# Optimization experiments

Hardware: AMD Instinct MI355X
Metric: run time of the kernel (lower is better)

The kernel has to match this reference:

```python
import jax, jax.numpy as jnp
import numpy as np

NUM_EMB = 8192
EMB_DIM = 512
SPAN = 8            # max_span == fixed_segment_size
COMMIT = 0.25
BOUND_W = 0.01


def setup_inputs() -> dict:
    key = jax.random.key(0)
    k_x, k_e, k_w = jax.random.split(key, 3)
    B, T, D = 16, 8192, EMB_DIM
    x = jax.random.normal(k_x, (B, T, D), dtype=jnp.float32)
    emb = jax.random.normal(k_e, (NUM_EMB, D), dtype=jnp.float32) * 0.02
    Wb = jax.random.normal(k_w, (D, 1), dtype=jnp.float32) * 0.02
    bb = jnp.zeros((1,), dtype=jnp.float32)
    return {"x": x, "emb": emb, "Wb": Wb, "bb": bb}


def reference(x, emb, Wb, bb):
    # Eval-mode forward of AdaptiveTemporalVQ (no gumbel sampling, no EMA update).
    B, T, D = x.shape
    # boundary predictor: Linear(D, 1) -> squeeze
    boundary_logits = (x @ Wb)[..., 0] + bb[0]                      # [B, T]
    boundaries = (jax.nn.sigmoid(boundary_logits) > 0.5).astype(x.dtype)

    num_segments = (T + SPAN - 1) // SPAN
    pad = num_segments * SPAN - T
    x_p = jnp.pad(x, ((0, 0), (0, pad), (0, 0))) if pad > 0 else x
    # temporal mean pooling over fixed segments
    pooled = x_p.reshape(B, num_segments, SPAN, D).mean(axis=2)      # [B, S, D]

    # --- VectorQuantizer ---
    flat = pooled.reshape(-1, D)                                     # [N, D]
    dist = (jnp.sum(flat ** 2, axis=1, keepdims=True)
            + jnp.sum(emb ** 2, axis=1)
            - 2.0 * flat @ emb.T)                                    # [N, K]
    idx = jnp.argmin(dist, axis=1)                                   # [N]
    quantized = emb[idx].reshape(B, num_segments, D)                 # codebook gather

    e_latent_loss = jnp.mean((jax.lax.stop_gradient(quantized) - pooled) ** 2)
    vq_loss = COMMIT * e_latent_loss
    # straight-through estimator
    q_st = pooled + jax.lax.stop_gradient(quantized - pooled)

    # expand each segment code back over its SPAN timesteps
    q_exp = jnp.broadcast_to(q_st[:, :, None, :], (B, num_segments, SPAN, D))
    quantized_out = q_exp.reshape(B, num_segments * SPAN, D)[:, :T, :]
    idx_seg = idx.reshape(B, num_segments)
    idx_out = jnp.broadcast_to(idx_seg[:, :, None], (B, num_segments, SPAN))
    idx_out = idx_out.reshape(B, num_segments * SPAN)[:, :T]

    target_rate = jnp.float32(1.0 / SPAN)
    boundary_loss = (boundaries.mean() - target_rate) ** 2
    total_loss = vq_loss + BOUND_W * boundary_loss
    return quantized_out, total_loss, idx_out, boundaries
```

## Files before the change

kernel.cpp:

```cpp
#include <hip/hip_runtime.h>

#define B_    16
#define T_    8192
#define D_    512
#define K_    8192
#define S_    1024
#define N_    16384
#define NBT   131072

#define LOSS_OFF 67108864
#define IDX_OFF  67108865
#define BND_OFF  67239937

typedef __bf16 bf16x8 __attribute__((ext_vector_type(8)));
typedef float  f32x4  __attribute__((ext_vector_type(4)));

__device__ __forceinline__ unsigned int fsort(float f){
  unsigned int u = __float_as_uint(f);
  return (u & 0x80000000u) ? ~u : (u | 0x80000000u);
}
__device__ __forceinline__ float funsort(unsigned int su){
  unsigned int u = (su & 0x80000000u) ? (su ^ 0x80000000u) : ~su;
  return __uint_as_float(u);
}
__device__ __forceinline__ unsigned short f2bf(float f){
  unsigned int u = __float_as_uint(f);
  return (unsigned short)((u + 0x7fffu + ((u >> 16) & 1u)) >> 16);
}
__device__ __forceinline__ void gload16(const void* g, void* l){
  __builtin_amdgcn_global_load_lds((const __attribute__((address_space(1))) void*)g,
                                   (__attribute__((address_space(3))) void*)l, 16, 0, 0);
}

__global__ void k_init(int* cnt){
  if(threadIdx.x == 0 && blockIdx.x == 0) *cnt = 0;
}

__global__ void k_embnorm(const float4* __restrict__ emb4, float* __restrict__ enorm,
                          unsigned short* __restrict__ embh){
  const int wid  = (blockIdx.x * blockDim.x + threadIdx.x) >> 6;
  const int lane = threadIdx.x & 63;
  float4 a = emb4[wid * 128 + (lane << 1)];
  float4 b = emb4[wid * 128 + (lane << 1) + 1];
  float s = a.x*a.x + a.y*a.y + a.z*a.z + a.w*a.w
          + b.x*b.x + b.y*b.y + b.z*b.z + b.w*b.w;
  #pragma unroll
  for(int off = 32; off; off >>= 1) s += __shfl_xor(s, off);
  if(lane == 0) enorm[wid] = s;
  unsigned short* dst = embh + ((size_t)wid << 9) + (lane << 3);
  *(ushort4*)(dst)     = make_ushort4(f2bf(a.x), f2bf(a.y), f2bf(a.z), f2bf(a.w));
  *(ushort4*)(dst + 4) = make_ushort4(f2bf(b.x), f2bf(b.y), f2bf(b.z), f2bf(b.w));
}

__launch_bounds__(256)
__global__ void k_prep(const float4* __restrict__ x4, const float4* __restrict__ wb4,
                       const float* __restrict__ bb, float4* __restrict__ pooled4,
                       unsigned short* __restrict__ pooledh, float* __restrict__ bnd,
                       int* __restrict__ cnt){
  __shared__ double ld[4][8][8];
  const int tid  = threadIdx.x;
  const int row0 = blockIdx.x << 5;
  const double bbv = (double)bb[0];
  #pragma unroll
  for(int it = 0; it < 2; it++){
    const int slot  = (it << 8) + tid;
    const int seg_l = slot >> 7;
    const int c4    = slot & 127;
    const float4 w  = wb4[c4];
    const float4* src = x4 + ((size_t)(row0 + (seg_l << 3)) * 128 + c4);
    float4 acc = src[0];
    double p[8];
    p[0] = (double)acc.x*w.x + (double)acc.y*w.y + (double)acc.z*w.z + (double)acc.w*w.w;
    #pragma unroll
    for(int t = 1; t < 8; t++){
      const float4 v = src[(size_t)t * 128];
      acc.x += v.x; acc.y += v.y; acc.z += v.z; acc.w += v.w;
      p[t] = (double)v.x*w.x + (double)v.y*w.y + (double)v.z*w.z + (double)v.w*w.w;
    }
    acc.x *= 0.125f; acc.y *= 0.125f; acc.z *= 0.125f; acc.w *= 0.125f;
    const int u = ((blockIdx.x << 2) + seg_l) * 128 + c4;
    pooled4[u] = acc;
    *(ushort4*)(pooledh + ((size_t)u << 2)) =
        make_ushort4(f2bf(acc.x), f2bf(acc.y), f2bf(acc.z), f2bf(acc.w));
    #pragma unroll
    for(int t = 0; t < 8; t++){
      #pragma unroll
      for(int off = 1; off < 16; off <<= 1) p[t] += __shfl_xor(p[t], off);
    }
    if((c4 & 15) == 0){
      #pragma unroll
      for(int t = 0; t < 8; t++) ld[seg_l][t][c4 >> 4] = p[t];
    }
  }
  __syncthreads();
  if(tid < 32){
    const double* q = ld[tid >> 3][tid & 7];
    double s = bbv;
    #pragma unroll
    for(int h = 0; h < 8; h++) s += q[h];
    const bool f = s > 0.0;
    bnd[row0 + tid] = f ? 1.0f : 0.0f;
    const unsigned long long m = __ballot(f);
    if(tid == 0) atomicAdd(cnt, (int)__popcll(m));
  }
}

__launch_bounds__(256, 4)
__global__ void k_distx(const unsigned short* __restrict__ Ah,
                        const unsigned short* __restrict__ Bh,
                        const float* __restrict__ enorm,
                        unsigned long long* __restrict__ cand64){
  __shared__ __align__(16) unsigned short sA[4096];
  __shared__ __align__(16) unsigned short sB[4096];
  const int tid  = threadIdx.x;
  const int w    = tid >> 6, lane = tid & 63;
  const int wm   = w >> 1,  wn   = w & 1;
  const int c    = lane & 15, q  = lane >> 4;

  const int bid   = blockIdx.x;
  const int st    = bid >> 9;
  const int loc   = bid & 511;
  const int row_t = (st << 3) + (loc & 7);
  const int col_t = loc >> 3;
  const int rowbase = row_t << 7;
  const int colbase = col_t << 7;

  f32x4 acc[4][4];
  #pragma unroll
  for(int i = 0; i < 4; i++)
    #pragma unroll
    for(int j = 0; j < 4; j++) acc[i][j] = (f32x4){0.f, 0.f, 0.f, 0.f};

  const int sr  = lane >> 2;
  const int skc = (lane & 3) << 3;

  const unsigned short* Ap0 = Ah + (size_t)(rowbase + w*32 + sr)      * 512 + skc;
  const unsigned short* Ap1 = Ah + (size_t)(rowbase + w*32 + 16 + sr) * 512 + skc;
  const unsigned short* Bp0 = Bh + (size_t)(colbase + w*32 + sr)      * 512 + skc;
  const unsigned short* Bp1 = Bh + (size_t)(colbase + w*32 + 16 + sr) * 512 + skc;
  unsigned short* lA0 = &sA[(w*32)      * 32];
  unsigned short* lA1 = &sA[(w*32 + 16) * 32];
  unsigned short* lB0 = &sB[(w*32)      * 32];
  unsigned short* lB1 = &sB[(w*32 + 16) * 32];

  for(int kb = 0; kb < 512; kb += 32){
    gload16(Ap0 + kb, lA0);
    gload16(Ap1 + kb, lA1);
    gload16(Bp0 + kb, lB0);
    gload16(Bp1 + kb, lB1);
    __syncthreads();
    bf16x8 af[4], bg[4];
    #pragma unroll
    for(int i = 0; i < 4; i++) af[i] = *(const bf16x8*)&sA[(wm*64 + i*16 + c)*32 + q*8];
    #pragma unroll
    for(int j = 0; j < 4; j++) bg[j] = *(const bf16x8*)&sB[(wn*64 + j*16 + c)*32 + q*8];
    #pragma unroll
    for(int i = 0; i < 4; i++)
      #pragma unroll
      for(int j = 0; j < 4; j++)
        acc[i][j] = __builtin_amdgcn_mfma_f32_16x16x32_bf16(af[i], bg[j], acc[i][j], 0, 0, 0);
    __syncthreads();
  }

  float en[4];
  #pragma unroll
  for(int j = 0; j < 4; j++) en[j] = enorm[colbase + wn*64 + j*16 + c];

  #pragma unroll
  for(int i = 0; i < 4; i++){
    #pragma unroll
    for(int r = 0; r < 4; r++){
      unsigned int k1 = 0xffffffffu, k2 = 0xffffffffu;
      #pragma unroll
      for(int j = 0; j < 4; j++){
        const float d = fmaf(-2.0f, acc[i][j][r], en[j]);
        const unsigned int col = (unsigned int)(colbase + wn*64 + j*16 + c);
        const unsigned int key = (fsort(d) & 0xffffe000u) | col;
        if(key < k1){ k2 = k1; k1 = key; } else if(key < k2){ k2 = key; }
      }
      #pragma unroll
      for(int off = 1; off < 4; off <<= 1){
        const unsigned int o1 = __shfl_xor(k1, off);
        const unsigned int o2 = __shfl_xor(k2, off);
        if(o1 < k1){ k2 = min(k1, o2); k1 = o1; }
        else       { k2 = min(k2, o1); }
      }
      if((c & 3) == 0){
        const int row = rowbase + wm*64 + i*16 + (q << 2) + r;
        const int g   = (col_t << 3) + (wn << 2) + (c >> 2);
        cand64[(size_t)row * 512 + g] = ((unsigned long long)k2 << 32) | k1;
      }
    }
  }
}

__launch_bounds__(256)
__global__ void k_fixup(const float* __restrict__ pooled, const float* __restrict__ emb,
                        const unsigned int* __restrict__ cand,
                        int* __restrict__ idxf, double* __restrict__ part){
  const int lane = threadIdx.x & 63, wv = threadIdx.x >> 6;
  const int row = (blockIdx.x << 2) + wv;
  const uint4* cr = (const uint4*)(cand + ((size_t)row << 10));
  unsigned int ks[16];
  #pragma unroll
  for(int m = 0; m < 4; m++){
    const uint4 v = cr[m*64 + lane];
    ks[m*4+0] = v.x; ks[m*4+1] = v.y; ks[m*4+2] = v.z; ks[m*4+3] = v.w;
  }
  unsigned int mn = 0xffffffffu;
  #pragma unroll
  for(int g = 0; g < 16; g++) mn = min(mn, ks[g]);
  #pragma unroll
  for(int off = 32; off; off >>= 1) mn = min(mn, (unsigned int)__shfl_xor(mn, off));
  const float thr = funsort(mn & 0xffffe000u) + 0.01f;

  double bestd = 1e300; int besti = 0x7fffffff;
  const float4* p4 = (const float4*)(pooled + ((size_t)row << 9));
  const float4 pa = p4[lane << 1], pb = p4[(lane << 1) + 1];
  #pragma unroll
  for(int g = 0; g < 16; g++){
    const bool flag = funsort(ks[g] & 0xffffe000u) <= thr;
    unsigned long long mask = __ballot(flag);
    while(mask){
      const int l = __ffsll(mask) - 1;
      mask &= mask - 1;
      const int code = (int)(__shfl(ks[g], l) & 0x1fffu);
      const float4* e4 = (const float4*)(emb + ((size_t)code << 9));
      const float4 ea = e4[lane << 1], eb = e4[(lane << 1) + 1];
      double s = 0.0, d;
      d = (double)pa.x - ea.x; s += d * d;  d = (double)pa.y - ea.y; s += d * d;
      d = (double)pa.z - ea.z; s += d * d;  d = (double)pa.w - ea.w; s += d * d;
      d = (double)pb.x - eb.x; s += d * d;  d = (double)pb.y - eb.y; s += d * d;
      d = (double)pb.z - eb.z; s += d * d;  d = (double)pb.w - eb.w; s += d * d;
      #pragma unroll
      for(int off = 32; off; off >>= 1) s += __shfl_xor(s, off);
      if(s < bestd || (s == bestd && code < besti)){ bestd = s; besti = code; }
    }
  }
  __shared__ double se[4];
  if(lane == 0){ idxf[row] = besti; se[wv] = bestd; }
  __syncthreads();
  if(threadIdx.x == 0) part[blockIdx.x] = se[0] + se[1] + se[2] + se[3];
}

__global__ void k_loss(const double* __restrict__ part, const int* __restrict__ cnt,
                       float* __restrict__ out_loss){
  const int tid = threadIdx.x;
  double s = 0.0;
  for(int i = tid; i < 4096; i += 256) s += part[i];
  #pragma unroll
  for(int off = 32; off; off >>= 1) s += __shfl_xor(s, off);
  __shared__ double sb[4];
  if((tid & 63) == 0) sb[tid >> 6] = s;
  __syncthreads();
  if(tid == 0){
    const double e  = sb[0] + sb[1] + sb[2] + sb[3];
    const double el = e / (double)((size_t)N_ * 512);
    const double bm = (double)(*cnt) / 131072.0 - 0.125;
    const double loss = 0.25 * el + 0.01 * bm * bm;
    *out_loss = (float)loss;
  }
}

__launch_bounds__(256)
__global__ void k_expand(const float4* __restrict__ emb4, const int* __restrict__ idxf,
                         float4* __restrict__ q4, float* __restrict__ idxo){
  const int lane = threadIdx.x & 63, wv = threadIdx.x >> 6;
  const int seg = (blockIdx.x << 2) + wv;
  const int idx = idxf[seg];
  const float4 a = emb4[idx * 128 + (lane << 1)];
  const float4 b = emb4[idx * 128 + (lane << 1) + 1];
  float4* dst = q4 + ((size_t)seg << 10);
  #pragma unroll
  for(int t = 0; t < 8; t++){
    dst[t * 128 + (lane << 1)]     = a;
    dst[t * 128 + (lane << 1) + 1] = b;
  }
  if(lane < 8) idxo[(seg << 3) + lane] = (float)idx;
}

extern "C" void kernel_launch(void* const* d_in, const int* in_sizes, int n_in,
                              void* d_out, int out_size, void* d_ws, size_t ws_size,
                              hipStream_t stream){
  const float* x   = (const float*)d_in[0];
  const float* emb = (const float*)d_in[1];
  const float* wb  = (const float*)d_in[2];
  const float* bb  = (const float*)d_in[3];
  float* out = (float*)d_out;

  char* ws = (char*)d_ws;
  int*    cnt   = (int*)(ws + 0);
  double* part  = (double*)(ws + 64);
  float*  enorm = (float*)(ws + 32832);
  int*    idxf  = (int*)(ws + 65600);

  float*              pooled  = (float*)d_out;
  unsigned long long* cand64  = (unsigned long long*)((char*)d_out + (48ull  << 20));
  unsigned short*     pooledh = (unsigned short*)((char*)d_out + (112ull << 20));
  unsigned short*     embh    = (unsigned short*)((char*)d_out + (128ull << 20));

  float* bnd   = out + BND_OFF;
  float* idxo  = out + IDX_OFF;
  float* lossp = out + LOSS_OFF;

  hipLaunchKernelGGL(k_init,    dim3(1),     dim3(64),  0, stream, cnt);
  hipLaunchKernelGGL(k_embnorm, dim3(2048),  dim3(256), 0, stream, (const float4*)emb, enorm, embh);
  hipLaunchKernelGGL(k_prep,    dim3(4096),  dim3(256), 0, stream, (const float4*)x, (const float4*)wb,
                     bb, (float4*)pooled, pooledh, bnd, cnt);
  hipLaunchKernelGGL(k_distx,   dim3(8192),  dim3(256), 0, stream, pooledh, embh, enorm, cand64);
  hipLaunchKernelGGL(k_fixup,   dim3(4096),  dim3(256), 0, stream, pooled, emb, (const unsigned int*)cand64, idxf, part);
  hipLaunchKernelGGL(k_loss,    dim3(1),     dim3(256), 0, stream, part, cnt, lossp);
  hipLaunchKernelGGL(k_expand,  dim3(4096),  dim3(256), 0, stream, (const float4*)emb, idxf, (float4*)d_out, idxo);
}
```

Measured before the change: 702.0 us.

## Reduce distance candidates fully per wave-column and remap blocks per XCD

```diff
diff --git a/kernel.cpp b/kernel.cpp
--- a/kernel.cpp
+++ b/kernel.cpp
@@ -32,12 +32,9 @@
                                    (__attribute__((address_space(3))) void*)l, 16, 0, 0);
 }
 
-__global__ void k_init(int* cnt){
-  if(threadIdx.x == 0 && blockIdx.x == 0) *cnt = 0;
-}
-
 __global__ void k_embnorm(const float4* __restrict__ emb4, float* __restrict__ enorm,
-                          unsigned short* __restrict__ embh){
+                          unsigned short* __restrict__ embh, int* __restrict__ cnt){
+  if(blockIdx.x == 0 && threadIdx.x == 0) *cnt = 0;
   const int wid  = (blockIdx.x * blockDim.x + threadIdx.x) >> 6;
   const int lane = threadIdx.x & 63;
   float4 a = emb4[wid * 128 + (lane << 1)];
@@ -118,10 +115,10 @@
   const int c    = lane & 15, q  = lane >> 4;
 
   const int bid   = blockIdx.x;
-  const int st    = bid >> 9;
-  const int loc   = bid & 511;
-  const int row_t = (st << 3) + (loc & 7);
-  const int col_t = loc >> 3;
+  const int xcd   = bid & 7;
+  const int local = bid >> 3;
+  const int row_t = (xcd << 4) + (local & 15);
+  const int col_t = local >> 4;
   const int rowbase = row_t << 7;
   const int colbase = col_t << 7;
 
@@ -179,16 +176,16 @@
         if(key < k1){ k2 = k1; k1 = key; } else if(key < k2){ k2 = key; }
       }
       #pragma unroll
-      for(int off = 1; off < 4; off <<= 1){
+      for(int off = 1; off < 16; off <<= 1){
         const unsigned int o1 = __shfl_xor(k1, off);
         const unsigned int o2 = __shfl_xor(k2, off);
         if(o1 < k1){ k2 = min(k1, o2); k1 = o1; }
         else       { k2 = min(k2, o1); }
       }
-      if((c & 3) == 0){
+      if(c == 0){
         const int row = rowbase + wm*64 + i*16 + (q << 2) + r;
-        const int g   = (col_t << 3) + (wn << 2) + (c >> 2);
-        cand64[(size_t)row * 512 + g] = ((unsigned long long)k2 << 32) | k1;
+        cand64[((size_t)row << 7) + (col_t << 1) + wn] =
+            ((unsigned long long)k2 << 32) | k1;
       }
     }
   }
@@ -196,20 +193,16 @@
 
 __launch_bounds__(256)
 __global__ void k_fixup(const float* __restrict__ pooled, const float* __restrict__ emb,
-                        const unsigned int* __restrict__ cand,
+                        const unsigned long long* __restrict__ cand64,
                         int* __restrict__ idxf, double* __restrict__ part){
   const int lane = threadIdx.x & 63, wv = threadIdx.x >> 6;
   const int row = (blockIdx.x << 2) + wv;
-  const uint4* cr = (const uint4*)(cand + ((size_t)row << 10));
-  unsigned int ks[16];
-  #pragma unroll
-  for(int m = 0; m < 4; m++){
-    const uint4 v = cr[m*64 + lane];
-    ks[m*4+0] = v.x; ks[m*4+1] = v.y; ks[m*4+2] = v.z; ks[m*4+3] = v.w;
-  }
-  unsigned int mn = 0xffffffffu;
-  #pragma unroll
-  for(int g = 0; g < 16; g++) mn = min(mn, ks[g]);
+  const ulonglong2* cr = (const ulonglong2*)(cand64 + ((size_t)row << 7));
+  const ulonglong2 v = cr[lane];
+  unsigned int ks[4];
+  ks[0] = (unsigned int)v.x; ks[1] = (unsigned int)(v.x >> 32);
+  ks[2] = (unsigned int)v.y; ks[3] = (unsigned int)(v.y >> 32);
+  unsigned int mn = min(min(ks[0], ks[1]), min(ks[2], ks[3]));
   #pragma unroll
   for(int off = 32; off; off >>= 1) mn = min(mn, (unsigned int)__shfl_xor(mn, off));
   const float thr = funsort(mn & 0xffffe000u) + 0.01f;
@@ -218,7 +211,7 @@
   const float4* p4 = (const float4*)(pooled + ((size_t)row << 9));
   const float4 pa = p4[lane << 1], pb = p4[(lane << 1) + 1];
   #pragma unroll
-  for(int g = 0; g < 16; g++){
+  for(int g = 0; g < 4; g++){
     const bool flag = funsort(ks[g] & 0xffffe000u) <= thr;
     unsigned long long mask = __ballot(flag);
     while(mask){
@@ -296,19 +289,18 @@
 
   float*              pooled  = (float*)d_out;
   unsigned long long* cand64  = (unsigned long long*)((char*)d_out + (48ull  << 20));
-  unsigned short*     pooledh = (unsigned short*)((char*)d_out + (112ull << 20));
-  unsigned short*     embh    = (unsigned short*)((char*)d_out + (128ull << 20));
+  unsigned short*     pooledh = (unsigned short*)((char*)d_out + (80ull  << 20));
+  unsigned short*     embh    = (unsigned short*)((char*)d_out + (100ull << 20));
 
   float* bnd   = out + BND_OFF;
   float* idxo  = out + IDX_OFF;
   float* lossp = out + LOSS_OFF;
 
-  hipLaunchKernelGGL(k_init,    dim3(1),     dim3(64),  0, stream, cnt);
-  hipLaunchKernelGGL(k_embnorm, dim3(2048),  dim3(256), 0, stream, (const float4*)emb, enorm, embh);
+  hipLaunchKernelGGL(k_embnorm, dim3(2048),  dim3(256), 0, stream, (const float4*)emb, enorm, embh, cnt);
   hipLaunchKernelGGL(k_prep,    dim3(4096),  dim3(256), 0, stream, (const float4*)x, (const float4*)wb,
                      bb, (float4*)pooled, pooledh, bnd, cnt);
   hipLaunchKernelGGL(k_distx,   dim3(8192),  dim3(256), 0, stream, pooledh, embh, enorm, cand64);
-  hipLaunchKernelGGL(k_fixup,   dim3(4096),  dim3(256), 0, stream, pooled, emb, (const unsigned int*)cand64, idxf, part);
+  hipLaunchKernelGGL(k_fixup,   dim3(4096),  dim3(256), 0, stream, pooled, emb, cand64, idxf, part);
   hipLaunchKernelGGL(k_loss,    dim3(1),     dim3(256), 0, stream, part, cnt, lossp);
   hipLaunchKernelGGL(k_expand,  dim3(4096),  dim3(256), 0, stream, (const float4*)emb, idxf, (float4*)d_out, idxo);
 }
```

Result: no change. 697.3 us (-0.7%).
